# Kernel optimization log

Hardware: AMD Instinct MI355X
Metric: run time of the kernel (lower is better)

The kernel has to match this reference:

```python
import jax, jax.numpy as jnp
import numpy as np

B, T, DIM, H = 2, 2048, 1024, 16
HD = DIM // H  # head_dim = 64
ROPE_BASE = 10000.0


def setup_inputs() -> dict:
    key = jax.random.key(0)
    k1, k2, k3, k4 = jax.random.split(key, 4)
    s = 1.0 / np.sqrt(DIM)
    return {
        "x": jax.random.normal(k1, (B, T, DIM), dtype=jnp.float32),
        "Wqkv": jax.random.normal(k2, (DIM, 3 * DIM), dtype=jnp.float32) * s,
        "Wout": jax.random.normal(k3, (DIM, DIM), dtype=jnp.float32) * s,
        "bout": jax.random.normal(k4, (DIM,), dtype=jnp.float32) * 0.01,
    }


def _rotate_half(x):
    # interleaved rotation: (x0,x1,x2,x3,...) -> (-x1,x0,-x3,x2,...)
    x1 = x[..., ::2]
    x2 = x[..., 1::2]
    return jnp.stack((-x2, x1), axis=-1).reshape(x.shape)


def _rope_cos_sin(seq_len, dtype):
    inv_freq = 1.0 / (ROPE_BASE ** (jnp.arange(0, HD, 2, dtype=jnp.float32) / HD))
    t = jnp.arange(seq_len, dtype=jnp.float32)
    freqs = t[:, None] * inv_freq[None, :]          # [T, HD/2]
    emb = jnp.concatenate((freqs, freqs), axis=-1)  # [T, HD] (cat layout, as in source)
    return jnp.cos(emb).astype(dtype), jnp.sin(emb).astype(dtype)


def reference(x, Wqkv, Wout, bout):
    b, t, _ = x.shape
    qkv = x @ Wqkv                                  # [B, T, 3*DIM]
    q, k, v = jnp.split(qkv, 3, axis=-1)
    # b t (h d) -> b h t d
    reshape = lambda z: z.reshape(b, t, H, HD).transpose(0, 2, 1, 3)
    q, k, v = reshape(q), reshape(k), reshape(v)
    cos, sin = _rope_cos_sin(t, x.dtype)            # [T, HD]
    q = q * cos + _rotate_half(q) * sin
    k = k * cos + _rotate_half(k) * sin
    scale = HD ** -0.5
    scores = jnp.einsum("bhqd,bhkd->bhqk", q, k) * scale
    attn = jax.nn.softmax(scores, axis=-1)
    out = jnp.einsum("bhqk,bhkd->bhqd", attn, v)    # [B, H, T, HD]
    out = out.transpose(0, 2, 1, 3).reshape(b, t, DIM)
    return out @ Wout + bout
```

## Files before the change

### kernel.cpp

```cpp
#include <hip/hip_runtime.h>
#include <math.h>


typedef unsigned short u16;
typedef __attribute__((ext_vector_type(8))) short short8;
typedef __attribute__((ext_vector_type(4))) short short4v;
typedef __attribute__((ext_vector_type(4))) float f32x4;
typedef __attribute__((ext_vector_type(16))) float f32x16;

#define T_SEQ 2048

#if __has_builtin(__builtin_amdgcn_exp2f)
#define EXP2(x) __builtin_amdgcn_exp2f(x)
#else
#define EXP2(x) exp2f(x)
#endif

__device__ __forceinline__ float b2f(u16 u) {
    union { unsigned int i; float f; } x; x.i = ((unsigned int)u) << 16; return x.f;
}
__device__ __forceinline__ u16 f2b(float f) {
    union { float f; unsigned int i; } x; x.f = f;
    return (u16)((x.i + 0x7FFFu + ((x.i >> 16) & 1u)) >> 16);
}
__device__ __forceinline__ void gl_lds16(const u16* g, u16* l) {
    __builtin_amdgcn_global_load_lds(
        (const __attribute__((address_space(1))) unsigned int*)g,
        (__attribute__((address_space(3))) unsigned int*)l, 16, 0, 0);
}
__device__ __forceinline__ short4v pack4(float a, float b, float c, float d) {
    union { float f; unsigned int u; } xa, xb, xc, xd;
    xa.f = a; xb.f = b; xc.f = c; xd.f = d;
    union { unsigned int u2[2]; short4v s; } r;
    r.u2[0] = (xa.u >> 16) | (xb.u & 0xffff0000u);
    r.u2[1] = (xc.u >> 16) | (xd.u & 0xffff0000u);
    return r.s;
}

__global__ __launch_bounds__(256) void setup_kernel(
    const float* __restrict__ x, const float* __restrict__ Wqkv,
    const float* __restrict__ Wout, u16* __restrict__ xb,
    u16* __restrict__ WqkvT, u16* __restrict__ WoutT,
    float* __restrict__ costab, float* __restrict__ sintab)
{
    const int bid = blockIdx.x;
    const int tid = threadIdx.x;

    if (bid < 4096) {
        int i = (bid * 256 + tid) * 4;
        float4 v = *(const float4*)(x + i);
        ushort4 w;
        w.x = f2b(v.x); w.y = f2b(v.y); w.z = f2b(v.z); w.w = f2b(v.w);
        *(ushort4*)(xb + i) = w;
        return;
    }
    if (bid < 8192) {
        const float* in; u16* out; int R, Cn, bx, by;
        if (bid < 7168) { in = Wqkv; out = WqkvT; R = 1024; Cn = 3072;
                          int id = bid - 4096; bx = id % 96; by = id / 96; }
        else            { in = Wout; out = WoutT; R = 1024; Cn = 1024;
                          int id = bid - 7168; bx = id & 31; by = id >> 5; }
        __shared__ u16 tile[32][33];
        const int tx = tid & 31, ty = tid >> 5;
        const int r0 = by * 32, c0 = bx * 32;
#pragma unroll
        for (int rr = ty; rr < 32; rr += 8)
            tile[tx][rr] = f2b(in[(size_t)(r0 + rr) * Cn + c0 + tx]);
        __syncthreads();
#pragma unroll
        for (int rr = ty; rr < 32; rr += 8)
            out[(size_t)(c0 + rr) * R + r0 + tx] = tile[rr][tx];
        return;
    }
    {
        int idx = (bid - 8192) * 256 + tid;
        int t = idx >> 6, d = idx & 63;
        const float nl32 = -0.28782313662425576f;
        float f = __expf((float)(d & 31) * nl32);
        float s, c;
        __sincosf((float)t * f, &s, &c);
        costab[idx] = c; sintab[idx] = s;
    }
}

template<int OBF>
__global__ __launch_bounds__(256) void gemm_bt_mfma(
    const u16* __restrict__ A, const u16* __restrict__ Bt,
    void* __restrict__ Cv, const float* __restrict__ bias,
    int M, int N, int K)
{
    __shared__ u16 As[128 * 32];
    __shared__ u16 Bs[128 * 32];

    const int tid = threadIdx.x;
    const int wave = tid >> 6, lane = tid & 63;
    const int col = lane & 15, quad = lane >> 4;
    const int wm = (wave & 1) * 64, wn = (wave >> 1) * 64;
    const int m0 = blockIdx.y * 128, n0 = blockIdx.x * 128;

    f32x4 acc[4][4];
#pragma unroll
    for (int i = 0; i < 4; ++i)
#pragma unroll
        for (int j = 0; j < 4; ++j) acc[i][j] = f32x4{0.f, 0.f, 0.f, 0.f};

    const int c1 = tid, c2 = tid + 256;
    const u16* a1 = A + (size_t)(m0 + (c1 >> 2)) * K + (c1 & 3) * 8;
    const u16* a2 = A + (size_t)(m0 + (c2 >> 2)) * K + (c2 & 3) * 8;
    const u16* b1 = Bt + (size_t)(n0 + (c1 >> 2)) * K + (c1 & 3) * 8;
    const u16* b2 = Bt + (size_t)(n0 + (c2 >> 2)) * K + (c2 & 3) * 8;
    u16* la1 = As + c1 * 8; u16* la2 = As + c2 * 8;
    u16* lb1 = Bs + c1 * 8; u16* lb2 = Bs + c2 * 8;

    for (int k0 = 0; k0 < K; k0 += 32) {
        __syncthreads();
        gl_lds16(a1 + k0, la1);
        gl_lds16(a2 + k0, la2);
        gl_lds16(b1 + k0, lb1);
        gl_lds16(b2 + k0, lb2);
        __syncthreads();

        short8 af[4], bfr[4];
#pragma unroll
        for (int i = 0; i < 4; ++i) {
            af[i]  = *(const short8*)&As[(wm + i * 16 + col) * 32 + quad * 8];
            bfr[i] = *(const short8*)&Bs[(wn + i * 16 + col) * 32 + quad * 8];
        }
#pragma unroll
        for (int i = 0; i < 4; ++i)
#pragma unroll
            for (int j = 0; j < 4; ++j)
                acc[i][j] = __builtin_amdgcn_mfma_f32_16x16x32_bf16(
                    af[i], bfr[j], acc[i][j], 0, 0, 0);
    }

#pragma unroll
    for (int j = 0; j < 4; ++j) {
        int n = n0 + wn + j * 16 + col;
        float bv = bias ? bias[n] : 0.f;
#pragma unroll
        for (int i = 0; i < 4; ++i) {
            int mbase = m0 + wm + i * 16 + quad * 4;
#pragma unroll
            for (int r = 0; r < 4; ++r) {
                if (OBF) ((u16*)Cv)[(size_t)(mbase + r) * N + n] = f2b(acc[i][j][r] + bv);
                else     ((float*)Cv)[(size_t)(mbase + r) * N + n] = acc[i][j][r] + bv;
            }
        }
    }
}

__global__ __launch_bounds__(256) void prep_kernel(
    const u16* __restrict__ qkvb, const float* __restrict__ costab,
    const float* __restrict__ sintab, u16* __restrict__ Qb,
    u16* __restrict__ Kb, u16* __restrict__ Vimg)
{
    __shared__ u16 Vls[64][72];

    const int tid = threadIdx.x;
    const int bh = blockIdx.y;
    const int t0 = blockIdx.x * 64;
    const int b = bh >> 4, h = bh & 15;
    const int t_loc = tid >> 2;
    const int d0 = (tid & 3) * 16;

    const int t = t0 + t_loc;
    const u16* qp = qkvb + ((size_t)(b * T_SEQ + t)) * 3072 + h * 64 + d0;

    float ct[16], st[16];
    {
        const float* cp = costab + (size_t)t * 64 + d0;
        const float* sp = sintab + (size_t)t * 64 + d0;
#pragma unroll
        for (int j = 0; j < 16; j += 4) {
            *(float4*)&ct[j] = *(const float4*)(cp + j);
            *(float4*)&st[j] = *(const float4*)(sp + j);
        }
    }

#pragma unroll
    for (int part = 0; part < 2; ++part) {
        const float sc = part ? 1.f : 0.18033688011112042f;
        const u16* src = qp + part * 1024;
        u16* dst = (part ? Kb : Qb) + ((size_t)(bh * T_SEQ + t)) * 64 + d0;
        short8 v0 = *(const short8*)(src);
        short8 v1 = *(const short8*)(src + 8);
        float f[16];
#pragma unroll
        for (int j = 0; j < 8; ++j) { f[j] = b2f((u16)v0[j]); f[8 + j] = b2f((u16)v1[j]); }
        u16 o[16];
#pragma unroll
        for (int i = 0; i < 8; ++i) {
            float e = f[2 * i], od = f[2 * i + 1];
            o[2 * i]     = f2b((e * ct[2 * i]      - od * st[2 * i]) * sc);
            o[2 * i + 1] = f2b((od * ct[2 * i + 1] + e  * st[2 * i + 1]) * sc);
        }
        *(short8*)(dst)     = *(short8*)&o[0];
        *(short8*)(dst + 8) = *(short8*)&o[8];
    }

    {
        const u16* src = qp + 2048;
        *(short8*)&Vls[t_loc][d0]     = *(const short8*)(src);
        *(short8*)&Vls[t_loc][d0 + 8] = *(const short8*)(src + 8);
    }
    __syncthreads();
    {
        const int dt    = tid >> 7;
        const int g     = (tid >> 5) & 3;
        const int hi2   = (tid >> 4) & 1;
        const int dpair = tid & 15;
        const int kl0 = g * 8 + hi2 * 4;
        const int d0v = dt * 32 + 2 * dpair;
        const int kt_base = blockIdx.x * 2;
#pragma unroll
        for (int ktl = 0; ktl < 2; ++ktl) {
            u16 o[8];
#pragma unroll
            for (int j = 0; j < 4; ++j) {
                o[j]     = Vls[ktl * 32 + kl0 + j][d0v];
                o[4 + j] = Vls[ktl * 32 + kl0 + j][d0v + 1];
            }
            u16* dst = Vimg + ((size_t)(bh * 64 + kt_base + ktl)) * 2048 + tid * 8;
            *(short8*)dst = *(short8*)&o[0];
        }
    }
}

__global__ __launch_bounds__(256, 4) void attn32_kernel(
    const u16* __restrict__ Qb, const u16* __restrict__ Kb,
    const u16* __restrict__ Vimg, float* __restrict__ po, float* __restrict__ pl)
{
    __shared__ u16 Kbuf[3][2048];
    __shared__ u16 Vbuf[3][2048];

    const int tid = threadIdx.x;
    const int wave = tid >> 6, lane = tid & 63;
    const int qcol = lane & 31;
    const int hi = lane >> 5;

    const int bid = blockIdx.x;
    const int lbid = (bid & 7) * 128 + (bid >> 3);
    const int bh = lbid >> 5;
    const int seg = (lbid >> 4) & 1;
    const int qblk = lbid & 15;
    const int qrow0 = qblk * 128 + wave * 32;

    short8 qa[4];
    {
        const u16* qp = Qb + ((size_t)(bh * T_SEQ + qrow0 + qcol)) * 64 + hi * 8;
#pragma unroll
        for (int c = 0; c < 4; ++c) qa[c] = *(const short8*)(qp + c * 16);
    }

    f32x16 O0, O1;
#pragma unroll
    for (int i = 0; i < 16; ++i) { O0[i] = 0.f; O1[i] = 0.f; }
    float Lacc = 0.f;

    const u16* kg_ptr = Kb + ((size_t)bh * T_SEQ + qcol) * 64 + wave * 16 + hi * 8;
    const u16* vg_ptr = Vimg + ((size_t)bh * 64) * 2048 + tid * 8;

    const int kt0 = seg * 32;

#define STAGE(p, rr) do {                                                     \
        gl_lds16(kg_ptr + (size_t)(kt0 + (rr)) * 2048, &Kbuf[p][tid * 8]);    \
        gl_lds16(vg_ptr + (size_t)(kt0 + (rr)) * 2048, &Vbuf[p][tid * 8]);    \
    } while (0)

    STAGE(0, 0);
    STAGE(1, 1);

    int cur = 0, prv = 2;
    for (int r = 0; r < 32; ++r) {
        if (r < 31) asm volatile("s_waitcnt vmcnt(2)" ::: "memory");
        else        asm volatile("s_waitcnt vmcnt(0)" ::: "memory");
        __builtin_amdgcn_s_barrier();
        asm volatile("" ::: "memory");
        __builtin_amdgcn_sched_barrier(0);

        short8 kf[4];
        short4v vv[8];
#pragma unroll
        for (int f = 0; f < 4; ++f)
            kf[f] = *(const short8*)&Kbuf[cur][(f * 64 + lane) * 8];
#pragma unroll
        for (int g = 0; g < 4; ++g) {
            vv[2 * g]     = *(const short4v*)&Vbuf[cur][g * 256 + lane * 4];
            vv[2 * g + 1] = *(const short4v*)&Vbuf[cur][1024 + g * 256 + lane * 4];
        }

        if (r < 30) STAGE(prv, r + 2);

        f32x16 sT;
#pragma unroll
        for (int ii = 0; ii < 16; ++ii) sT[ii] = 0.f;
        __builtin_amdgcn_s_setprio(1);
#pragma unroll
        for (int c = 0; c < 4; ++c)
            sT = __builtin_amdgcn_mfma_f32_32x32x16_bf16(kf[c], qa[c], sT, 0, 0, 0);
        __builtin_amdgcn_s_setprio(0);

        float pe[16];
#pragma unroll
        for (int ii = 0; ii < 16; ++ii) pe[ii] = EXP2(sT[ii]);
        short4v pb[4];
#pragma unroll
        for (int g = 0; g < 4; ++g) {
            pb[g] = pack4(pe[4 * g + 0], pe[4 * g + 1],
                          pe[4 * g + 2], pe[4 * g + 3]);
            Lacc += (pe[4 * g + 0] + pe[4 * g + 1]) +
                    (pe[4 * g + 2] + pe[4 * g + 3]);
        }

        __builtin_amdgcn_s_setprio(1);
#pragma unroll
        for (int g = 0; g < 4; ++g) {
            O0 = __builtin_amdgcn_mfma_f32_32x32x8bf16_1k(vv[2 * g],     pb[g], O0, 0, 0, 0);
            O1 = __builtin_amdgcn_mfma_f32_32x32x8bf16_1k(vv[2 * g + 1], pb[g], O1, 0, 0, 0);
        }
        __builtin_amdgcn_s_setprio(0);

        prv = cur;
        cur = (cur == 2) ? 0 : cur + 1;
    }
#undef STAGE

    float Lq = Lacc + __shfl(Lacc, lane ^ 32);

    const size_t prow = ((size_t)(seg * 32 + bh)) * T_SEQ + qrow0 + qcol;
    float* op = po + prow * 64;
#pragma unroll
    for (int g2 = 0; g2 < 4; ++g2) {
        int dd = g2 * 8 + hi * 4;
        *(float4*)(op + dd)      = make_float4(O0[4 * g2 + 0], O0[4 * g2 + 1],
                                               O0[4 * g2 + 2], O0[4 * g2 + 3]);
        *(float4*)(op + 32 + dd) = make_float4(O1[4 * g2 + 0], O1[4 * g2 + 1],
                                               O1[4 * g2 + 2], O1[4 * g2 + 3]);
    }
    if (hi == 0) pl[prow] = Lq;
}

__global__ __launch_bounds__(256) void attn_combine_kernel(
    const float* __restrict__ po, const float* __restrict__ pl,
    u16* __restrict__ aob)
{
    const int idx = blockIdx.x * 256 + (int)threadIdx.x;
    const int row = idx >> 4;
    const int d4 = idx & 15;

    float4 o0 = *(const float4*)(po + (size_t)row * 64 + d4 * 4);
    float4 o1 = *(const float4*)(po + ((size_t)row + 65536) * 64 + d4 * 4);
    float L = pl[row] + pl[row + 65536];
    float inv = 1.f / L;

    const int bh = row >> 11, t = row & 2047;
    const int b = bh >> 4, h = bh & 15;
    ushort4 w;
    w.x = f2b((o0.x + o1.x) * inv);
    w.y = f2b((o0.y + o1.y) * inv);
    w.z = f2b((o0.z + o1.z) * inv);
    w.w = f2b((o0.w + o1.w) * inv);
    *(ushort4*)(aob + ((size_t)(b * T_SEQ + t)) * 1024 + h * 64 + d4 * 4) = w;
}

extern "C" void kernel_launch(void* const* d_in, const int* in_sizes, int n_in,
                              void* d_out, int out_size, void* d_ws, size_t ws_size,
                              hipStream_t stream)
{
    const float* x    = (const float*)d_in[0];
    const float* Wqkv = (const float*)d_in[1];
    const float* Wout = (const float*)d_in[2];
    const float* bout = (const float*)d_in[3];
    float* out = (float*)d_out;

    char* w = (char*)d_ws;
    u16* qkvb    = (u16*)(w);
    u16* xb      = (u16*)(w + 25165824);
    u16* WqkvT   = (u16*)(w + 33554432);
    u16* WoutT   = (u16*)(w + 39845888);
    u16* aob     = (u16*)(w + 41943040);
    u16* Qb      = (u16*)(w + 50331648);
    u16* Kb      = (u16*)(w + 58720256);
    u16* Vimg    = (u16*)(w + 67108864);
    float* ctab  = (float*)(w + 75497472);
    float* stab  = (float*)(w + 76021760);
    float* po    = (float*)(w);
    float* pl    = (float*)(w + 33554432);

    dim3 blk(256);
    setup_kernel<<<dim3(8704), blk, 0, stream>>>(x, Wqkv, Wout, xb, WqkvT, WoutT, ctab, stab);
    gemm_bt_mfma<1><<<dim3(24, 32), blk, 0, stream>>>(xb, WqkvT, qkvb, nullptr, 4096, 3072, 1024);
    prep_kernel<<<dim3(32, 32), blk, 0, stream>>>(qkvb, ctab, stab, Qb, Kb, Vimg);
    attn32_kernel<<<dim3(1024), blk, 0, stream>>>(Qb, Kb, Vimg, po, pl);
    attn_combine_kernel<<<dim3(4096), blk, 0, stream>>>(po, pl, aob);
    gemm_bt_mfma<0><<<dim3(8, 32), blk, 0, stream>>>(aob, WoutT, out, bout, 4096, 1024, 1024);
}
```

Before: 211.9 us.

## Drop split-KV attention, fuse normalization, use 32x32x16 MFMA for PV via permlane swap

Each attention block now walks all 64 key tiles instead of half, so the partial-output buffers and the separate combine kernel go away and normalization plus bf16 store happen in the epilogue. The V image layout is rewritten so the PV product can use the wider 32x32x16 bf16 MFMA, with P operands rearranged across half-waves by v_permlane32_swap. Launch bounds drop to 2 blocks per SM, and the grid halves to 512 blocks, which may leave CUs underfilled.

```diff
diff --git a/kernel.cpp b/kernel.cpp
--- a/kernel.cpp
+++ b/kernel.cpp
@@ -28,13 +28,9 @@
         (const __attribute__((address_space(1))) unsigned int*)g,
         (__attribute__((address_space(3))) unsigned int*)l, 16, 0, 0);
 }
-__device__ __forceinline__ short4v pack4(float a, float b, float c, float d) {
-    union { float f; unsigned int u; } xa, xb, xc, xd;
-    xa.f = a; xb.f = b; xc.f = c; xd.f = d;
-    union { unsigned int u2[2]; short4v s; } r;
-    r.u2[0] = (xa.u >> 16) | (xb.u & 0xffff0000u);
-    r.u2[1] = (xc.u >> 16) | (xd.u & 0xffff0000u);
-    return r.s;
+__device__ __forceinline__ unsigned int packpair(float a, float b) {
+    union { float f; unsigned int u; } xa, xb; xa.f = a; xb.f = b;
+    return (xa.u >> 16) | (xb.u & 0xffff0000u);
 }
 
 __global__ __launch_bounds__(256) void setup_kernel(
@@ -206,30 +202,28 @@
     }
     __syncthreads();
     {
-        const int dt    = tid >> 7;
-        const int g     = (tid >> 5) & 3;
-        const int hi2   = (tid >> 4) & 1;
-        const int dpair = tid & 15;
-        const int kl0 = g * 8 + hi2 * 4;
-        const int d0v = dt * 32 + 2 * dpair;
+        const int m_  = (tid >> 7) & 1;
+        const int db  = (tid >> 6) & 1;
+        const int h2  = (tid >> 5) & 1;
+        const int dv  = tid & 31;
+        const int k0v = m_ * 16 + h2 * 8;
+        const int dcol = db * 32 + dv;
         const int kt_base = blockIdx.x * 2;
 #pragma unroll
         for (int ktl = 0; ktl < 2; ++ktl) {
             u16 o[8];
 #pragma unroll
-            for (int j = 0; j < 4; ++j) {
-                o[j]     = Vls[ktl * 32 + kl0 + j][d0v];
-                o[4 + j] = Vls[ktl * 32 + kl0 + j][d0v + 1];
-            }
+            for (int j = 0; j < 8; ++j)
+                o[j] = Vls[ktl * 32 + k0v + j][dcol];
             u16* dst = Vimg + ((size_t)(bh * 64 + kt_base + ktl)) * 2048 + tid * 8;
             *(short8*)dst = *(short8*)&o[0];
         }
     }
 }
 
-__global__ __launch_bounds__(256, 4) void attn32_kernel(
+__global__ __launch_bounds__(256, 2) void attn32_kernel(
     const u16* __restrict__ Qb, const u16* __restrict__ Kb,
-    const u16* __restrict__ Vimg, float* __restrict__ po, float* __restrict__ pl)
+    const u16* __restrict__ Vimg, u16* __restrict__ aob)
 {
     __shared__ u16 Kbuf[3][2048];
     __shared__ u16 Vbuf[3][2048];
@@ -240,9 +234,8 @@
     const int hi = lane >> 5;
 
     const int bid = blockIdx.x;
-    const int lbid = (bid & 7) * 128 + (bid >> 3);
-    const int bh = lbid >> 5;
-    const int seg = (lbid >> 4) & 1;
+    const int lbid = (bid & 7) * 64 + (bid >> 3);
+    const int bh = lbid >> 4;
     const int qblk = lbid & 15;
     const int qrow0 = qblk * 128 + wave * 32;
 
@@ -261,36 +254,31 @@
     const u16* kg_ptr = Kb + ((size_t)bh * T_SEQ + qcol) * 64 + wave * 16 + hi * 8;
     const u16* vg_ptr = Vimg + ((size_t)bh * 64) * 2048 + tid * 8;
 
-    const int kt0 = seg * 32;
-
 #define STAGE(p, rr) do {                                                     \
-        gl_lds16(kg_ptr + (size_t)(kt0 + (rr)) * 2048, &Kbuf[p][tid * 8]);    \
-        gl_lds16(vg_ptr + (size_t)(kt0 + (rr)) * 2048, &Vbuf[p][tid * 8]);    \
+        gl_lds16(kg_ptr + (size_t)(rr) * 2048, &Kbuf[p][tid * 8]);            \
+        gl_lds16(vg_ptr + (size_t)(rr) * 2048, &Vbuf[p][tid * 8]);            \
     } while (0)
 
     STAGE(0, 0);
     STAGE(1, 1);
 
     int cur = 0, prv = 2;
-    for (int r = 0; r < 32; ++r) {
-        if (r < 31) asm volatile("s_waitcnt vmcnt(2)" ::: "memory");
+    for (int r = 0; r < 64; ++r) {
+        if (r < 63) asm volatile("s_waitcnt vmcnt(2)" ::: "memory");
         else        asm volatile("s_waitcnt vmcnt(0)" ::: "memory");
         __builtin_amdgcn_s_barrier();
         asm volatile("" ::: "memory");
         __builtin_amdgcn_sched_barrier(0);
 
-        short8 kf[4];
-        short4v vv[8];
+        short8 kf[4], vA[4];
 #pragma unroll
         for (int f = 0; f < 4; ++f)
             kf[f] = *(const short8*)&Kbuf[cur][(f * 64 + lane) * 8];
 #pragma unroll
-        for (int g = 0; g < 4; ++g) {
-            vv[2 * g]     = *(const short4v*)&Vbuf[cur][g * 256 + lane * 4];
-            vv[2 * g + 1] = *(const short4v*)&Vbuf[cur][1024 + g * 256 + lane * 4];
-        }
-
-        if (r < 30) STAGE(prv, r + 2);
+        for (int rg = 0; rg < 4; ++rg)
+            vA[rg] = *(const short8*)&Vbuf[cur][rg * 512 + lane * 8];
+
+        if (r < 62) STAGE(prv, r + 2);
 
         f32x16 sT;
 #pragma unroll
@@ -304,21 +292,34 @@
         float pe[16];
 #pragma unroll
         for (int ii = 0; ii < 16; ++ii) pe[ii] = EXP2(sT[ii]);
-        short4v pb[4];
-#pragma unroll
-        for (int g = 0; g < 4; ++g) {
-            pb[g] = pack4(pe[4 * g + 0], pe[4 * g + 1],
-                          pe[4 * g + 2], pe[4 * g + 3]);
+#pragma unroll
+        for (int g = 0; g < 4; ++g)
             Lacc += (pe[4 * g + 0] + pe[4 * g + 1]) +
                     (pe[4 * g + 2] + pe[4 * g + 3]);
-        }
+
+        unsigned int W0 = packpair(pe[0],  pe[1]);
+        unsigned int W1 = packpair(pe[2],  pe[3]);
+        unsigned int W2 = packpair(pe[4],  pe[5]);
+        unsigned int W3 = packpair(pe[6],  pe[7]);
+        unsigned int W4 = packpair(pe[8],  pe[9]);
+        unsigned int W5 = packpair(pe[10], pe[11]);
+        unsigned int W6 = packpair(pe[12], pe[13]);
+        unsigned int W7 = packpair(pe[14], pe[15]);
+
+        asm volatile("v_permlane32_swap_b32 %0, %1" : "+v"(W0), "+v"(W2));
+        asm volatile("v_permlane32_swap_b32 %0, %1" : "+v"(W1), "+v"(W3));
+        asm volatile("v_permlane32_swap_b32 %0, %1" : "+v"(W4), "+v"(W6));
+        asm volatile("v_permlane32_swap_b32 %0, %1" : "+v"(W5), "+v"(W7));
+
+        union FU { unsigned int u[4]; short8 s; } f0, f1;
+        f0.u[0] = W0; f0.u[1] = W1; f0.u[2] = W2; f0.u[3] = W3;
+        f1.u[0] = W4; f1.u[1] = W5; f1.u[2] = W6; f1.u[3] = W7;
 
         __builtin_amdgcn_s_setprio(1);
-#pragma unroll
-        for (int g = 0; g < 4; ++g) {
-            O0 = __builtin_amdgcn_mfma_f32_32x32x8bf16_1k(vv[2 * g],     pb[g], O0, 0, 0, 0);
-            O1 = __builtin_amdgcn_mfma_f32_32x32x8bf16_1k(vv[2 * g + 1], pb[g], O1, 0, 0, 0);
-        }
+        O0 = __builtin_amdgcn_mfma_f32_32x32x16_bf16(vA[0], f0.s, O0, 0, 0, 0);
+        O1 = __builtin_amdgcn_mfma_f32_32x32x16_bf16(vA[1], f0.s, O1, 0, 0, 0);
+        O0 = __builtin_amdgcn_mfma_f32_32x32x16_bf16(vA[2], f1.s, O0, 0, 0, 0);
+        O1 = __builtin_amdgcn_mfma_f32_32x32x16_bf16(vA[3], f1.s, O1, 0, 0, 0);
         __builtin_amdgcn_s_setprio(0);
 
         prv = cur;
@@ -327,41 +328,21 @@
 #undef STAGE
 
     float Lq = Lacc + __shfl(Lacc, lane ^ 32);
-
-    const size_t prow = ((size_t)(seg * 32 + bh)) * T_SEQ + qrow0 + qcol;
-    float* op = po + prow * 64;
+    float inv = 1.f / Lq;
+
+    const int b = bh >> 4, h = bh & 15;
+    u16* ab = aob + ((size_t)(b * T_SEQ + qrow0 + qcol)) * 1024 + h * 64;
 #pragma unroll
     for (int g2 = 0; g2 < 4; ++g2) {
         int dd = g2 * 8 + hi * 4;
-        *(float4*)(op + dd)      = make_float4(O0[4 * g2 + 0], O0[4 * g2 + 1],
-                                               O0[4 * g2 + 2], O0[4 * g2 + 3]);
-        *(float4*)(op + 32 + dd) = make_float4(O1[4 * g2 + 0], O1[4 * g2 + 1],
-                                               O1[4 * g2 + 2], O1[4 * g2 + 3]);
-    }
-    if (hi == 0) pl[prow] = Lq;
-}
-
-__global__ __launch_bounds__(256) void attn_combine_kernel(
-    const float* __restrict__ po, const float* __restrict__ pl,
-    u16* __restrict__ aob)
-{
-    const int idx = blockIdx.x * 256 + (int)threadIdx.x;
-    const int row = idx >> 4;
-    const int d4 = idx & 15;
-
-    float4 o0 = *(const float4*)(po + (size_t)row * 64 + d4 * 4);
-    float4 o1 = *(const float4*)(po + ((size_t)row + 65536) * 64 + d4 * 4);
-    float L = pl[row] + pl[row + 65536];
-    float inv = 1.f / L;
-
-    const int bh = row >> 11, t = row & 2047;
-    const int b = bh >> 4, h = bh & 15;
-    ushort4 w;
-    w.x = f2b((o0.x + o1.x) * inv);
-    w.y = f2b((o0.y + o1.y) * inv);
-    w.z = f2b((o0.z + o1.z) * inv);
-    w.w = f2b((o0.w + o1.w) * inv);
-    *(ushort4*)(aob + ((size_t)(b * T_SEQ + t)) * 1024 + h * 64 + d4 * 4) = w;
+        ushort4 w0, w1;
+        w0.x = f2b(O0[4 * g2 + 0] * inv); w0.y = f2b(O0[4 * g2 + 1] * inv);
+        w0.z = f2b(O0[4 * g2 + 2] * inv); w0.w = f2b(O0[4 * g2 + 3] * inv);
+        w1.x = f2b(O1[4 * g2 + 0] * inv); w1.y = f2b(O1[4 * g2 + 1] * inv);
+        w1.z = f2b(O1[4 * g2 + 2] * inv); w1.w = f2b(O1[4 * g2 + 3] * inv);
+        *(ushort4*)(ab + dd)      = w0;
+        *(ushort4*)(ab + 32 + dd) = w1;
+    }
 }
 
 extern "C" void kernel_launch(void* const* d_in, const int* in_sizes, int n_in,
@@ -385,14 +366,11 @@
     u16* Vimg    = (u16*)(w + 67108864);
     float* ctab  = (float*)(w + 75497472);
     float* stab  = (float*)(w + 76021760);
-    float* po    = (float*)(w);
-    float* pl    = (float*)(w + 33554432);
 
     dim3 blk(256);
     setup_kernel<<<dim3(8704), blk, 0, stream>>>(x, Wqkv, Wout, xb, WqkvT, WoutT, ctab, stab);
     gemm_bt_mfma<1><<<dim3(24, 32), blk, 0, stream>>>(xb, WqkvT, qkvb, nullptr, 4096, 3072, 1024);
     prep_kernel<<<dim3(32, 32), blk, 0, stream>>>(qkvb, ctab, stab, Qb, Kb, Vimg);
-    attn32_kernel<<<dim3(1024), blk, 0, stream>>>(Qb, Kb, Vimg, po, pl);
-    attn_combine_kernel<<<dim3(4096), blk, 0, stream>>>(po, pl, aob);
+    attn32_kernel<<<dim3(512), blk, 0, stream>>>(Qb, Kb, Vimg, aob);
     gemm_bt_mfma<0><<<dim3(8, 32), blk, 0, stream>>>(aob, WoutT, out, bout, 4096, 1024, 1024);
 }
```

Result: faster. 199.2 us (-6.0%).
